# Optimization experiments

Measured on AMD Instinct MI355X. Metric: run time of the kernel, lower is better.

## Reference

```python
import jax, jax.numpy as jnp
import numpy as np
from jax import lax

T, B = 64, 16
N, W, R = 256, 64, 4          # mem_slot, mem_size, read_heads
IN, OUT = 64, 64
NHID, NNOUT = 256, 256
IF_SIZE = W * R + 3 * W + 5 * R + 3  # 471
EPS = 1e-6


def setup_inputs() -> dict:
    key = jax.random.key(0)
    ks = jax.random.split(key, 8)
    in_dim = IN + R * W
    def glorot(k, shape):
        fan_in = shape[0]
        return jax.random.normal(k, shape, dtype=jnp.float32) / np.sqrt(fan_in)
    return {
        "input_data": jax.random.normal(ks[0], (T, B, IN), dtype=jnp.float32),
        "W1": glorot(ks[1], (in_dim, NHID)),
        "b1": jnp.zeros((NHID,), jnp.float32),
        "W2": glorot(ks[2], (NHID, NNOUT)),
        "b2": jnp.zeros((NNOUT,), jnp.float32),
        "W_if": glorot(ks[3], (NNOUT, IF_SIZE)),
        "b_if": jnp.zeros((IF_SIZE,), jnp.float32),
        "W_out": glorot(ks[4], (NNOUT, OUT)),
        "W_mem_out": glorot(ks[5], (R * W, OUT)),
    }


def oneplus(x):
    return 1.0 + jax.nn.softplus(x)


def content_address(mem, keys, strengths):
    # mem [B,N,W], keys [B,W,R], strengths [B,R] -> weights [B,N,R]
    mem_n = mem / (jnp.linalg.norm(mem, axis=-1, keepdims=True) + EPS)
    key_n = keys / (jnp.linalg.norm(keys, axis=1, keepdims=True) + EPS)
    sim = jnp.einsum('bnw,bwr->bnr', mem_n, key_n)
    return jax.nn.softmax(sim * strengths[:, None, :], axis=1)


def parse_interface(z):
    # z: [B, IF_SIZE] -> dict of interface components (NeuCom layout)
    o = 0
    read_keys = z[:, o:o + W * R].reshape(-1, W, R); o += W * R
    read_str = oneplus(z[:, o:o + R]); o += R
    write_key = z[:, o:o + W]; o += W
    write_str = oneplus(z[:, o:o + 1]); o += 1
    erase = jax.nn.sigmoid(z[:, o:o + W]); o += W
    write_vec = z[:, o:o + W]; o += W
    free_gates = jax.nn.sigmoid(z[:, o:o + R]); o += R
    alloc_gate = jax.nn.sigmoid(z[:, o:o + 1]); o += 1
    write_gate = jax.nn.sigmoid(z[:, o:o + 1]); o += 1
    read_modes = jax.nn.softmax(z[:, o:o + 3 * R].reshape(-1, 3, R), axis=1)
    return (read_keys, read_str, write_key, write_str, erase, write_vec,
            free_gates, alloc_gate, write_gate, read_modes)


def _dnc_forward(input_data, W1, b1, W2, b2, W_if, b_if, W_out, W_mem_out):
    Bz = input_data.shape[1]
    eye = jnp.eye(N, dtype=input_data.dtype)

    def step(carry, x_t):
        mem, usage, rw, ww, prec, link, rvec = carry
        # --- controller (feedforward) ---
        ctrl_in = jnp.concatenate([x_t, rvec.reshape(Bz, R * W)], axis=1)
        h = jnp.tanh(ctrl_in @ W1 + b1)
        nn_out = jnp.tanh(h @ W2 + b2)
        (read_keys, read_str, write_key, write_str, erase, write_vec,
         free_gates, alloc_gate, write_gate, read_modes) = parse_interface(nn_out @ W_if + b_if)
        # --- write ---
        retention = jnp.prod(1.0 - free_gates[:, None, :] * rw, axis=2)   # [B,N]
        usage = (usage + ww - usage * ww) * retention
        idx = jnp.argsort(usage, axis=1)                                  # ascending usage
        u_sorted = jnp.take_along_axis(usage, idx, axis=1)
        prod_excl = jnp.concatenate(
            [jnp.ones((Bz, 1), usage.dtype), jnp.cumprod(u_sorted, axis=1)[:, :-1]], axis=1)
        alloc_sorted = (1.0 - u_sorted) * prod_excl
        alloc = jnp.take_along_axis(alloc_sorted, jnp.argsort(idx, axis=1), axis=1)
        wc = content_address(mem, write_key[:, :, None], write_str)[:, :, 0]  # [B,N]
        ww = write_gate * (alloc_gate * alloc + (1.0 - alloc_gate) * wc)
        mem = mem * (1.0 - ww[:, :, None] * erase[:, None, :]) \
              + ww[:, :, None] * write_vec[:, None, :]
        link = (1.0 - ww[:, :, None] - ww[:, None, :]) * link \
               + ww[:, :, None] * prec[:, None, :]
        link = link * (1.0 - eye)
        prec = (1.0 - jnp.sum(ww, axis=1, keepdims=True)) * prec + ww
        # --- read ---
        rc = content_address(mem, read_keys, read_str)                    # [B,N,R]
        fwd_w = jnp.einsum('bnm,bmr->bnr', link, rw)
        bwd_w = jnp.einsum('bmn,bmr->bnr', link, rw)
        rw = (bwd_w * read_modes[:, 0][:, None, :]
              + rc * read_modes[:, 1][:, None, :]
              + fwd_w * read_modes[:, 2][:, None, :])
        rvec = jnp.einsum('bnw,bnr->bwr', mem, rw)                        # [B,W,R]
        out = nn_out @ W_out + rvec.reshape(Bz, R * W) @ W_mem_out
        view = (free_gates, alloc_gate, write_gate, rw, ww, usage)
        return (mem, usage, rw, ww, prec, link, rvec), (out, view)

    carry0 = (
        jnp.full((Bz, N, W), EPS, input_data.dtype),   # mem_mat
        jnp.zeros((Bz, N), input_data.dtype),          # usage
        jnp.zeros((Bz, N, R), input_data.dtype),       # read_weight
        jnp.zeros((Bz, N), input_data.dtype),          # write_weight
        jnp.zeros((Bz, N), input_data.dtype),          # precedence
        jnp.zeros((Bz, N, N), input_data.dtype),       # link matrix
        jnp.zeros((Bz, W, R), input_data.dtype),       # read vectors
    )
    _, (outputs, _view) = lax.scan(step, carry0, input_data)
    return outputs  # [T,B,OUT]


def reference(input_data, W1, b1, W2, b2, W_if, b_if, W_out, W_mem_out):
    return _dnc_forward(input_data, W1, b1, W2, b2, W_if, b_if, W_out, W_mem_out)
```

## Files before the change

### kernel.cpp

```cpp
#include <hip/hip_runtime.h>
#include <hip/hip_fp16.h>
#include <math.h>

#define Tt 64
#define Bb 16
#define Nn 256
#define Ww 64
#define Rr 4
#define INd 64
#define OUTd 64
#define IFS 471
#define EPSf 1e-6f

#define W1OFF   0
#define W2OFF   40960
#define WIFOFF  73728
#define WOUTOFF 134016
#define WMEMOFF 142208
#define WTOT    150400

#define LROW    129
#define LINKB   (256 * LROW * 4)
#define SCRB    16384
#define FIXF    3824
#define SMEM_MAIN (LINKB + SCRB + FIXF * 4)
#define SMEM_FB   (SCRB + FIXF * 4)

typedef _Float16 h2v __attribute__((ext_vector_type(2)));
__device__ __forceinline__ float fdot2(__half2 a, __half2 b, float c) {
    return __builtin_amdgcn_fdot2(*(h2v*)&a, *(h2v*)&b, c, false);
}
__device__ __forceinline__ __half2 pkh(float a, float b) {
    auto r = __builtin_amdgcn_cvt_pkrtz(a, b);
    return *(__half2*)&r;
}

__device__ __forceinline__ float sigm(float x) { return 1.f / (1.f + expf(-x)); }
__device__ __forceinline__ float oneplus_(float x) {
    return 1.f + fmaxf(x, 0.f) + log1pf(expf(-fabsf(x)));
}
__device__ __forceinline__ float wsum(float v) {
#pragma unroll
    for (int o = 32; o; o >>= 1) v += __shfl_xor(v, o, 64);
    return v;
}
__device__ __forceinline__ float wmaxr(float v) {
#pragma unroll
    for (int o = 32; o; o >>= 1) v = fmaxf(v, __shfl_xor(v, o, 64));
    return v;
}

__device__ __attribute__((noinline)) float gemv_part(
    const __half2* __restrict__ wP, int str, int iters,
    const __half2* __restrict__ vin)
{
    float a[8] = {0.f,0.f,0.f,0.f,0.f,0.f,0.f,0.f};
#pragma unroll 1
    for (int j0 = 0; j0 < iters; j0 += 8) {
        __half2 hh[8], vv[8];
        int k8 = j0 >> 2;
        *(float4*)&hh[0] = *(const float4*)(wP + (size_t)k8 * str);
        *(float4*)&hh[4] = *(const float4*)(wP + (size_t)(k8 + 1) * str);
        *(float4*)&vv[0] = *(const float4*)(vin + j0);
        *(float4*)&vv[4] = *(const float4*)(vin + j0 + 4);
#pragma unroll
        for (int u = 0; u < 8; ++u) a[u] = fdot2(hh[u], vv[u], a[u]);
    }
    return ((a[0]+a[1])+(a[2]+a[3])) + ((a[4]+a[5])+(a[6]+a[7]));
}

__global__ void convert_weights(const float* __restrict__ W1, const float* __restrict__ W2,
                                const float* __restrict__ Wif, const float* __restrict__ Wout,
                                const float* __restrict__ Wmem, __half2* __restrict__ wp) {
    int i = blockIdx.x * blockDim.x + threadIdx.x;
    if (i >= WTOT) return;
    float a, b;
    if (i < W2OFF) {
        int q = i & 3, s = i >> 2, n = s & 255, k2 = (s >> 8) * 4 + q;
        a = W1[(2*k2)*256+n];  b = W1[(2*k2+1)*256+n];
    } else if (i < WIFOFF) {
        int t = i - W2OFF;
        int q = t & 3, s = t >> 2, n = s & 255, k2 = (s >> 8) * 4 + q;
        a = W2[(2*k2)*256+n];  b = W2[(2*k2+1)*256+n];
    } else if (i < WOUTOFF) {
        int t = i - WIFOFF;
        int q = t & 3, s = t >> 2, o = s % IFS, k2 = (s / IFS) * 4 + q;
        a = Wif[(2*k2)*IFS+o]; b = Wif[(2*k2+1)*IFS+o];
    } else if (i < WMEMOFF) {
        int t = i - WOUTOFF;
        int q = t & 3, s = t >> 2, n = s & 63, k2 = (s >> 6) * 4 + q;
        a = Wout[(2*k2)*64+n]; b = Wout[(2*k2+1)*64+n];
    } else {
        int t = i - WMEMOFF;
        int q = t & 3, s = t >> 2, n = s & 63, k2 = (s >> 6) * 4 + q;
        a = Wmem[(2*k2)*64+n]; b = Wmem[(2*k2+1)*64+n];
    }
    wp[i] = __floats2half2_rn(a, b);
}

template <bool LLINK>
__global__ __launch_bounds__(1024) void dnc_kernel(
    const float* __restrict__ x, const float* __restrict__ b1,
    const float* __restrict__ b2, const float* __restrict__ bif,
    const __half2* __restrict__ wp,
    __half* __restrict__ memg,
    __half2* __restrict__ linkg,
    float* __restrict__ out)
{
    extern __shared__ __align__(16) char smem[];
    const int b = blockIdx.x;
    const int tid = threadIdx.x;
    const int lane = tid & 63;
    const int wv = tid >> 6;

    __half2* l2p = (__half2*)smem;
    __half2* gl2 = linkg + (size_t)b * (256 * LROW);
    float* scr   = (float*)(smem + (LLINK ? LINKB : 0));
    __half* scrh = (__half*)scr;
    float* fx    = (float*)((char*)scr + SCRB);

    float*   s_rw    = fx + 0;
    __half2* s_ctrlh = (__half2*)(fx + 1024);
    __half2* s_hh    = (__half2*)(fx + 1184);
    __half2* s_nnh   = (__half2*)(fx + 1312);
    __half2* s_rwh   = (__half2*)(fx + 1440);
    float* s_z     = fx + 1952;
    float* s_usage = fx + 2424;
    float* s_ww    = fx + 2680;
    float* s_prec  = fx + 2936;
    float* s_wcdot = fx + 3192;
    float* s_wcss  = fx + 3448;
    float* s_knorm = fx + 3704;
    float* s_rstr  = fx + 3708;
    float* s_rmode = fx + 3712;
    float* s_sc    = fx + 3724;
    float* s_red   = fx + 3728;
    float* s_er    = fx + 3760;
    float* s_srt   = scr + 1024;
    float* s_cp    = scr + 1280;

    __half*  memh  = memg + (size_t)b * (Ww * Nn);
    __half2* memh2 = (__half2*)memh;

    auto lread = [&](int idx) -> __half2 {
        if constexpr (LLINK) return l2p[idx]; else return gl2[idx];
    };
    auto lwrite = [&](int idx, __half2 v) {
        if constexpr (LLINK) l2p[idx] = v; else gl2[idx] = v;
    };

    {
        __half2 z2 = pkh(0.f, 0.f);
#pragma unroll 1
        for (int i = tid; i < 256 * LROW; i += 1024) lwrite(i, z2);
        __half2 e2 = __floats2half2_rn(EPSf, EPSf);
#pragma unroll 1
        for (int j = 0; j < 8; ++j) memh2[tid + j * 1024] = e2;
        if (tid < 512) s_rwh[tid] = z2;
        if (tid < 32) {
            float2 xv = *(const float2*)&x[b * INd + 2 * tid];
            s_ctrlh[tid] = pkh(xv.x, xv.y);
        } else if (tid < 160) s_ctrlh[tid] = z2;
    }
    if (tid < 256) {
        s_usage[tid] = 0.f; s_ww[tid] = 0.f; s_prec[tid] = 0.f;
        s_rw[tid*4+0] = 0.f; s_rw[tid*4+1] = 0.f; s_rw[tid*4+2] = 0.f; s_rw[tid*4+3] = 0.f;
    }

#pragma unroll 1
    for (int t = 0; t < Tt; ++t) {
        __syncthreads();

        {
            int kc = wv >> 2, o = (wv & 3) * 64 + lane;
            scr[kc * 256 + o] = gemv_part(wp + W1OFF + o * 4 + kc * 10240, 1024, 40,
                                          s_ctrlh + kc * 40);
        }
        __syncthreads();
        if (tid < 256) {
            float v = tanhf(b1[tid] + ((scr[tid] + scr[256+tid]) + (scr[512+tid] + scr[768+tid])));
            float pv = __shfl_xor(v, 1, 64);
            if ((tid & 1) == 0) s_hh[tid >> 1] = pkh(v, pv);
        }
        __syncthreads();

        {
            int kc = wv >> 2, o = (wv & 3) * 64 + lane;
            scr[kc * 256 + o] = gemv_part(wp + W2OFF + o * 4 + kc * 8192, 1024, 32,
                                          s_hh + kc * 32);
        }
        __syncthreads();
        if (tid < 256) {
            float v = tanhf(b2[tid] + ((scr[tid] + scr[256+tid]) + (scr[512+tid] + scr[768+tid])));
            float pv = __shfl_xor(v, 1, 64);
            if ((tid & 1) == 0) s_nnh[tid >> 1] = pkh(v, pv);
        }
        __syncthreads();

        {
            int kc = wv >> 3, o = (wv & 7) * 64 + lane;
            if (o < IFS)
                scr[kc * 512 + o] = gemv_part(wp + WIFOFF + o * 4 + kc * 30144, 1884, 64,
                                              s_nnh + kc * 64);
        }
        __syncthreads();
        if (tid < IFS) s_z[tid] = bif[tid] + scr[tid] + scr[512 + tid];
        __syncthreads();

        if (wv < 4) {
            float vz = s_z[lane * 4 + wv];
            float s = wsum(vz * vz);
            if (lane == 0) s_knorm[wv] = sqrtf(s) + EPSf;
        } else if (wv == 4) {
            float vz = s_z[260 + lane];
            float s = wsum(vz * vz);
            if (lane == 0) s_sc[3] = sqrtf(s) + EPSf;
        } else if (wv == 5) {
            if (lane < 4) s_rstr[lane] = oneplus_(s_z[256 + lane]);
            else if (lane >= 8 && lane < 12) {
                int r = lane - 8;
                float a = s_z[459+r], bm = s_z[463+r], c = s_z[467+r];
                float mx = fmaxf(a, fmaxf(bm, c));
                float ea = expf(a-mx), eb = expf(bm-mx), ec = expf(c-mx);
                float inv = 1.f / ((ea+eb)+ec);
                s_rmode[0*4+r] = ea*inv; s_rmode[1*4+r] = eb*inv; s_rmode[2*4+r] = ec*inv;
            } else if (lane == 16) s_sc[0] = oneplus_(s_z[324]);
            else if (lane == 17) s_sc[1] = sigm(s_z[457]);
            else if (lane == 18) s_sc[2] = sigm(s_z[458]);
        } else if (wv == 6) {
            s_er[lane] = sigm(s_z[325 + lane]);
        } else if (wv >= 8 && wv < 12) {
            int n = tid - 512;
            float ret = 1.f;
#pragma unroll
            for (int r = 0; r < 4; ++r) {
                float fg = sigm(s_z[453 + r]);
                ret *= 1.f - fg * s_rw[n*4 + r];
            }
            float u = s_usage[n], wwo = s_ww[n];
            s_usage[n] = (u + wwo - u * wwo) * ret;
        } else if (wv >= 12) {
            int n = tid - 768;
            float dot = 0.f, ssv = 0.f;
#pragma unroll 1
            for (int w0 = 0; w0 < 64; w0 += 16) {
                __half hv[16];
#pragma unroll
                for (int u = 0; u < 16; ++u) hv[u] = memh[(w0 + u) * 256 + n];
#pragma unroll
                for (int u = 0; u < 16; ++u) {
                    float m = __half2float(hv[u]);
                    ssv = fmaf(m, m, ssv);
                    dot = fmaf(m, s_z[260 + w0 + u], dot);
                }
            }
            s_wcdot[n] = dot; s_wcss[n] = ssv;
        }
        __syncthreads();

        {
            int q = tid >> 8, n = tid & 255;
            float un = s_usage[n];
            float cnt = 0.f;
            int j0 = q * 64;
#pragma unroll 1
            for (int j = j0; j < j0 + 64; j += 4) {
                float4 uv = *(const float4*)&s_usage[j];
                cnt += (uv.x < un || (uv.x == un && j     < n)) ? 1.f : 0.f;
                cnt += (uv.y < un || (uv.y == un && j + 1 < n)) ? 1.f : 0.f;
                cnt += (uv.z < un || (uv.z == un && j + 2 < n)) ? 1.f : 0.f;
                cnt += (uv.w < un || (uv.w == un && j + 3 < n)) ? 1.f : 0.f;
            }
            scr[q * 256 + n] = cnt;
        }
        __syncthreads();

        if (wv == 0) {
            int rk[4]; float uu[4];
#pragma unroll
            for (int i = 0; i < 4; ++i) {
                int n = lane * 4 + i;
                float c = scr[n] + scr[256+n] + scr[512+n] + scr[768+n];
                rk[i] = (int)(c + 0.5f);
                uu[i] = s_usage[n];
                s_srt[rk[i]] = uu[i];
            }
            float4 vs = ((const float4*)s_srt)[lane];
            float p1 = vs.x * vs.y, p2 = p1 * vs.z, tot = p2 * vs.w;
            float incl = tot;
#pragma unroll
            for (int off = 1; off < 64; off <<= 1) {
                float tv = __shfl_up(incl, off, 64);
                if (lane >= off) incl *= tv;
            }
            float excl = __shfl_up(incl, 1, 64);
            if (lane == 0) excl = 1.f;
            float4 o4v; o4v.x = excl; o4v.y = excl*vs.x; o4v.z = excl*p1; o4v.w = excl*p2;
            ((float4*)s_cp)[lane] = o4v;

            float sims[4], mx = -1e30f;
#pragma unroll
            for (int i = 0; i < 4; ++i) {
                int n = lane * 4 + i;
                sims[i] = s_wcdot[n] / ((sqrtf(s_wcss[n]) + EPSf) * s_sc[3]) * s_sc[0];
                mx = fmaxf(mx, sims[i]);
            }
            mx = wmaxr(mx);
            float es[4], ls = 0.f;
#pragma unroll
            for (int i = 0; i < 4; ++i) { es[i] = expf(sims[i] - mx); ls += es[i]; }
            ls = wsum(ls);
            float ag = s_sc[1], wg = s_sc[2], inv = 1.f / ls, lw = 0.f;
#pragma unroll
            for (int i = 0; i < 4; ++i) {
                int n = lane * 4 + i;
                float alloc = (1.f - uu[i]) * s_cp[rk[i]];
                float wwn = wg * (ag * alloc + (1.f - ag) * es[i] * inv);
                s_ww[n] = wwn; lw += wwn;
            }
            lw = wsum(lw);
            if (lane == 0) s_red[0] = lw;
        }
        __syncthreads();

        if (tid < 512) {
            int kc = tid >> 7, p = tid & 127;
            int c0 = 2 * p, c1 = c0 + 1;
            float wwc0 = s_ww[c0], wwc1 = s_ww[c1];
            float pt0 = s_prec[c0], pt1 = s_prec[c1];
            float acc[8] = {0,0,0,0,0,0,0,0};
            int kbase = kc * 64;
#pragma unroll 1
            for (int k0 = kbase; k0 < kbase + 64; k0 += 8) {
                __half2 lv[8];
#pragma unroll
                for (int u = 0; u < 8; ++u) lv[u] = lread((k0 + u) * LROW + p);
                float wk8[8];
                *(float4*)&wk8[0] = *(const float4*)&s_ww[k0];
                *(float4*)&wk8[4] = *(const float4*)&s_ww[k0 + 4];
                float l0v[8], l1v[8];
#pragma unroll
                for (int u = 0; u < 8; ++u) {
                    int k = k0 + u;
                    float wk = wk8[u];
                    float2 lf = __half22float2(lv[u]);
                    float l0 = (1.f - wk - wwc0) * lf.x + wk * pt0;
                    float l1 = (1.f - wk - wwc1) * lf.y + wk * pt1;
                    if (k == c0) l0 = 0.f;
                    if (k == c1) l1 = 0.f;
                    l0v[u] = l0; l1v[u] = l1;
                }
#pragma unroll
                for (int u = 0; u < 8; ++u)
                    lwrite((k0 + u) * LROW + p, pkh(l0v[u], l1v[u]));
                __half2 l0p[4], l1p[4];
#pragma unroll
                for (int i = 0; i < 4; ++i) {
                    l0p[i] = pkh(l0v[2*i], l0v[2*i+1]);
                    l1p[i] = pkh(l1v[2*i], l1v[2*i+1]);
                }
                int kp0 = k0 >> 1;
#pragma unroll
                for (int r = 0; r < 4; ++r) {
                    __half2 rp[4];
                    *(float4*)rp = *(const float4*)(s_rwh + r * 128 + kp0);
#pragma unroll
                    for (int i = 0; i < 4; ++i) {
                        acc[r]     = fdot2(l0p[i], rp[i], acc[r]);
                        acc[4 + r] = fdot2(l1p[i], rp[i], acc[4 + r]);
                    }
                }
            }
            __half2* bp = (__half2*)scrh + (kc * 128 + p) * 4;
            bp[0] = pkh(acc[0], acc[1]);
            bp[1] = pkh(acc[2], acc[3]);
            bp[2] = pkh(acc[4], acc[5]);
            bp[3] = pkh(acc[6], acc[7]);
        } else {
            int t0 = tid - 512;
#pragma unroll 1
            for (int jb = 0; jb < 2; ++jb) {
                __half2 mv[8];
#pragma unroll
                for (int j = 0; j < 8; ++j) mv[j] = memh2[t0 + (jb * 8 + j) * 512];
#pragma unroll
                for (int j = 0; j < 8; ++j) {
                    int i2 = t0 + (jb * 8 + j) * 512;
                    int w = i2 >> 7, n2 = i2 & 127;
                    float er = s_er[w];
                    float wvv = s_z[389 + w];
                    float2 mf = __half22float2(mv[j]);
                    float wa = s_ww[2*n2], wb = s_ww[2*n2 + 1];
                    mf.x = mf.x * (1.f - wa * er) + wa * wvv;
                    mf.y = mf.y * (1.f - wb * er) + wb * wvv;
                    memh2[i2] = __floats2half2_rn(mf.x, mf.y);
                }
            }
        }
        __syncthreads();

        {
            int q = tid >> 8, n8 = tid & 255;
            float f[4] = {0.f, 0.f, 0.f, 0.f};
            int base = n8 * LROW + q * 32;
#pragma unroll 1
            for (int j0 = 0; j0 < 32; j0 += 8) {
                __half2 lv[8];
#pragma unroll
                for (int u = 0; u < 8; ++u) lv[u] = lread(base + j0 + u);
#pragma unroll
                for (int r = 0; r < 4; ++r) {
                    __half2 rp[8];
                    *(float4*)&rp[0] = *(const float4*)(s_rwh + r * 128 + q * 32 + j0);
                    *(float4*)&rp[4] = *(const float4*)(s_rwh + r * 128 + q * 32 + j0 + 4);
#pragma unroll
                    for (int u = 0; u < 8; ++u) f[r] = fdot2(lv[u], rp[u], f[r]);
                }
            }
            __half2* fp2 = (__half2*)(scrh + 4096) + (q * 256 + n8) * 2;
            fp2[0] = pkh(f[0], f[1]);
            fp2[1] = pkh(f[2], f[3]);
            if (q == 0) s_prec[n8] = (1.f - s_red[0]) * s_prec[n8] + s_ww[n8];
        }
        __syncthreads();

        int rr = tid >> 8, n8c = tid & 255;
        float bwv = 0.f, fwv = 0.f, e_rc = 0.f;
        {
#pragma unroll
            for (int kc = 0; kc < 4; ++kc)
                bwv += __half2float(scrh[(kc * 128 + (n8c >> 1)) * 8 + (n8c & 1) * 4 + rr]);
#pragma unroll
            for (int qq = 0; qq < 4; ++qq)
                fwv += __half2float(scrh[4096 + (qq * 256 + n8c) * 4 + rr]);
            float ssv = 0.f, dv = 0.f;
#pragma unroll 1
            for (int w0 = 0; w0 < 64; w0 += 16) {
                __half hv[16];
#pragma unroll
                for (int u = 0; u < 16; ++u) hv[u] = memh[(w0 + u) * 256 + n8c];
#pragma unroll
                for (int u = 0; u < 16; ++u) {
                    float m = __half2float(hv[u]);
                    ssv = fmaf(m, m, ssv);
                    dv = fmaf(m, s_z[(w0 + u) * 4 + rr], dv);
                }
            }
            float sim = dv / ((sqrtf(ssv) + EPSf) * s_knorm[rr]) * s_rstr[rr];
            e_rc = expf(sim);
            float s = wsum(e_rc);
            if (lane == 0) s_red[16 + wv] = s;
        }
        __syncthreads();
        {
            float sm = (s_red[16+rr*4+0] + s_red[16+rr*4+1]) + (s_red[16+rr*4+2] + s_red[16+rr*4+3]);
            float rc = e_rc / sm;
            float v = bwv * s_rmode[0*4+rr] + rc * s_rmode[1*4+rr] + fwv * s_rmode[2*4+rr];
            s_rw[n8c*4 + rr] = v;
            float pv = __shfl_xor(v, 1, 64);
            if ((n8c & 1) == 0) s_rwh[rr * 128 + (n8c >> 1)] = pkh(v, pv);
        }
        __syncthreads();

        {
            int kc = tid >> 8, o = tid & 255, w = o >> 2, r = o & 3;
            const __half2* mw2 = (const __half2*)(memh + w * 256 + kc * 64);
            const __half2* rw2 = s_rwh + r * 128 + kc * 32;
            float a = 0.f;
#pragma unroll
            for (int c = 0; c < 8; ++c) {
                __half2 mv[4], rv[4];
                *(float4*)mv = *(const float4*)(mw2 + c * 4);
                *(float4*)rv = *(const float4*)(rw2 + c * 4);
#pragma unroll
                for (int u = 0; u < 4; ++u) a = fdot2(mv[u], rv[u], a);
            }
            scr[kc * 256 + o] = a;
        }
        __syncthreads();

        if (tid < 256) {
            float v = (scr[tid] + scr[256+tid]) + (scr[512+tid] + scr[768+tid]);
            float pv = __shfl_xor(v, 1, 64);
            if ((tid & 1) == 0) s_ctrlh[32 + (tid >> 1)] = pkh(v, pv);
        } else if (tid >= 512 && tid < 544) {
            if (t + 1 < Tt) {
                int i = tid - 512;
                float2 xv = *(const float2*)&x[((t + 1) * Bb + b) * INd + 2 * i];
                s_ctrlh[i] = pkh(xv.x, xv.y);
            }
        }
        __syncthreads();

        {
            int c4 = wv, o4 = lane;
            const __half2* wsrc = (c4 < 8) ? (wp + WOUTOFF + o4 * 4 + c4 * 1024)
                                           : (wp + WMEMOFF + o4 * 4 + (c4 - 8) * 1024);
            const __half2* vsrc = (c4 < 8) ? (s_nnh + c4 * 16)
                                           : (s_ctrlh + 32 + (c4 - 8) * 16);
            scr[c4 * 64 + o4] = gemv_part(wsrc, 256, 16, vsrc);
        }
        __syncthreads();
        if (tid < 64) {
            float s = 0.f;
#pragma unroll
            for (int g = 0; g < 16; ++g) s += scr[g * 64 + tid];
            out[(t * Bb + b) * OUTd + tid] = s;
        }
    }
}

extern "C" void kernel_launch(void* const* d_in, const int* in_sizes, int n_in,
                              void* d_out, int out_size, void* d_ws, size_t ws_size,
                              hipStream_t stream) {
    const float* x    = (const float*)d_in[0];
    const float* W1   = (const float*)d_in[1];
    const float* b1   = (const float*)d_in[2];
    const float* W2   = (const float*)d_in[3];
    const float* b2   = (const float*)d_in[4];
    const float* Wif  = (const float*)d_in[5];
    const float* bif  = (const float*)d_in[6];
    const float* Wout = (const float*)d_in[7];
    const float* Wmem = (const float*)d_in[8];
    float* out = (float*)d_out;

    char* ws = (char*)d_ws;
    __half2* wp    = (__half2*)ws;
    __half*  memg  = (__half*)(ws + 601600);
    __half2* linkg = (__half2*)(ws + 601600 + 524288);

    convert_weights<<<dim3((WTOT + 255) / 256), dim3(256), 0, stream>>>(W1, W2, Wif, Wout, Wmem, wp);

    hipError_t rc = hipFuncSetAttribute(
        reinterpret_cast<const void*>(&dnc_kernel<true>),
        hipFuncAttributeMaxDynamicSharedMemorySize, SMEM_MAIN);
    if (rc == hipSuccess) {
        dnc_kernel<true><<<dim3(Bb), dim3(1024), SMEM_MAIN, stream>>>(
            x, b1, b2, bif, wp, memg, linkg, out);
    } else {
        dnc_kernel<false><<<dim3(Bb), dim3(1024), SMEM_FB, stream>>>(
            x, b1, b2, bif, wp, memg, linkg, out);
    }
}
```

Measured before the change: 1.999 ms.

## Keep a W-pair-interleaved half2 copy of memory for packed content-addressing dots

Adds a second global copy of the memory matrix stored as half2 pairs along the word dimension, maintained alongside the original during the write update. The two content-addressing loops (write key and read keys) now read half2 pairs and use packed fdot2 for both the dot product and the squared norm, with keys pre-packed into shared half2 buffers. The read-weight half buffer stride is padded to avoid conflicts, and some scratch arrays move into the scratch region. This halves the number of memory loads and converts scalar FMAs in addressing, at the cost of extra global writes per step and a larger workspace.

Result: faster. 1.880 ms (-5.9%).

```diff
diff --git a/kernel.cpp b/kernel.cpp
--- a/kernel.cpp
+++ b/kernel.cpp
@@ -22,9 +22,11 @@
 #define LROW    129
 #define LINKB   (256 * LROW * 4)
 #define SCRB    16384
-#define FIXF    3824
+#define FIXF    3456
 #define SMEM_MAIN (LINKB + SCRB + FIXF * 4)
 #define SMEM_FB   (SCRB + FIXF * 4)
+
+#define RWS 132
 
 typedef _Float16 h2v __attribute__((ext_vector_type(2)));
 __device__ __forceinline__ float fdot2(__half2 a, __half2 b, float c) {
@@ -104,6 +106,7 @@
     const float* __restrict__ b2, const float* __restrict__ bif,
     const __half2* __restrict__ wp,
     __half* __restrict__ memg,
+    __half2* __restrict__ memWg,
     __half2* __restrict__ linkg,
     float* __restrict__ out)
 {
@@ -124,23 +127,27 @@
     __half2* s_hh    = (__half2*)(fx + 1184);
     __half2* s_nnh   = (__half2*)(fx + 1312);
     __half2* s_rwh   = (__half2*)(fx + 1440);
-    float* s_z     = fx + 1952;
-    float* s_usage = fx + 2424;
-    float* s_ww    = fx + 2680;
-    float* s_prec  = fx + 2936;
-    float* s_wcdot = fx + 3192;
-    float* s_wcss  = fx + 3448;
-    float* s_knorm = fx + 3704;
-    float* s_rstr  = fx + 3708;
-    float* s_rmode = fx + 3712;
-    float* s_sc    = fx + 3724;
-    float* s_red   = fx + 3728;
-    float* s_er    = fx + 3760;
+    float* s_z     = fx + 1968;
+    float* s_usage = fx + 2440;
+    float* s_ww    = fx + 2696;
+    float* s_prec  = fx + 2952;
+    float* s_knorm = fx + 3208;
+    float* s_rstr  = fx + 3212;
+    float* s_rmode = fx + 3216;
+    float* s_sc    = fx + 3228;
+    float* s_red   = fx + 3232;
+    float* s_er    = fx + 3264;
+    __half2* s_keyh = (__half2*)(fx + 3328);
     float* s_srt   = scr + 1024;
     float* s_cp    = scr + 1280;
+    __half2* s_keyw2 = (__half2*)(scr + 1280);
+    float* s_wcdot = scr + 1536;
+    float* s_wcss  = scr + 1792;
 
     __half*  memh  = memg + (size_t)b * (Ww * Nn);
     __half2* memh2 = (__half2*)memh;
+    __half2* memW2 = memWg + (size_t)b * (32 * 256);
+    __half*  memWh = (__half*)memW2;
 
     auto lread = [&](int idx) -> __half2 {
         if constexpr (LLINK) return l2p[idx]; else return gl2[idx];
@@ -155,8 +162,8 @@
         for (int i = tid; i < 256 * LROW; i += 1024) lwrite(i, z2);
         __half2 e2 = __floats2half2_rn(EPSf, EPSf);
 #pragma unroll 1
-        for (int j = 0; j < 8; ++j) memh2[tid + j * 1024] = e2;
-        if (tid < 512) s_rwh[tid] = z2;
+        for (int j = 0; j < 8; ++j) { memh2[tid + j * 1024] = e2; memW2[tid + j * 1024] = e2; }
+        if (tid < 528) s_rwh[tid] = z2;
         if (tid < 32) {
             float2 xv = *(const float2*)&x[b * INd + 2 * tid];
             s_ctrlh[tid] = pkh(xv.x, xv.y);
@@ -204,7 +211,19 @@
                                               s_nnh + kc * 64);
         }
         __syncthreads();
-        if (tid < IFS) s_z[tid] = bif[tid] + scr[tid] + scr[512 + tid];
+        if (tid < IFS) {
+            float v = bif[tid] + scr[tid] + scr[512 + tid];
+            s_z[tid] = v;
+            float pv1 = __shfl_xor(v, 1, 64);
+            float pv4 = __shfl_xor(v, 4, 64);
+            if (tid < 256) {
+                if ((tid & 4) == 0)
+                    s_keyh[(tid & 3) * 32 + (tid >> 3)] = pkh(v, pv4);
+            } else if (tid >= 260 && tid < 324) {
+                if ((tid & 1) == 0)
+                    s_keyw2[(tid - 260) >> 1] = pkh(v, pv1);
+            }
+        }
         __syncthreads();
 
         if (wv < 4) {
@@ -241,17 +260,19 @@
             s_usage[n] = (u + wwo - u * wwo) * ret;
         } else if (wv >= 12) {
             int n = tid - 768;
+            const __half2* mW = memW2 + n;
             float dot = 0.f, ssv = 0.f;
 #pragma unroll 1
-            for (int w0 = 0; w0 < 64; w0 += 16) {
-                __half hv[16];
-#pragma unroll
-                for (int u = 0; u < 16; ++u) hv[u] = memh[(w0 + u) * 256 + n];
-#pragma unroll
-                for (int u = 0; u < 16; ++u) {
-                    float m = __half2float(hv[u]);
-                    ssv = fmaf(m, m, ssv);
-                    dot = fmaf(m, s_z[260 + w0 + u], dot);
+            for (int c = 0; c < 32; c += 8) {
+                __half2 mv[8], kv[8];
+#pragma unroll
+                for (int u = 0; u < 8; ++u) mv[u] = mW[(c + u) * 256];
+                *(float4*)&kv[0] = *(const float4*)(s_keyw2 + c);
+                *(float4*)&kv[4] = *(const float4*)(s_keyw2 + c + 4);
+#pragma unroll
+                for (int u = 0; u < 8; ++u) {
+                    ssv = fdot2(mv[u], mv[u], ssv);
+                    dot = fdot2(mv[u], kv[u], dot);
                 }
             }
             s_wcdot[n] = dot; s_wcss[n] = ssv;
@@ -363,7 +384,7 @@
 #pragma unroll
                 for (int r = 0; r < 4; ++r) {
                     __half2 rp[4];
-                    *(float4*)rp = *(const float4*)(s_rwh + r * 128 + kp0);
+                    *(float4*)rp = *(const float4*)(s_rwh + r * RWS + kp0);
 #pragma unroll
                     for (int i = 0; i < 4; ++i) {
                         acc[r]     = fdot2(l0p[i], rp[i], acc[r]);
@@ -393,7 +414,11 @@
                     float wa = s_ww[2*n2], wb = s_ww[2*n2 + 1];
                     mf.x = mf.x * (1.f - wa * er) + wa * wvv;
                     mf.y = mf.y * (1.f - wb * er) + wb * wvv;
-                    memh2[i2] = __floats2half2_rn(mf.x, mf.y);
+                    __half2 hv = __floats2half2_rn(mf.x, mf.y);
+                    memh2[i2] = hv;
+                    int wb2 = (w >> 1) * 512 + 4 * n2 + (w & 1);
+                    memWh[wb2]     = __low2half(hv);
+                    memWh[wb2 + 2] = __high2half(hv);
                 }
             }
         }
@@ -411,8 +436,8 @@
 #pragma unroll
                 for (int r = 0; r < 4; ++r) {
                     __half2 rp[8];
-                    *(float4*)&rp[0] = *(const float4*)(s_rwh + r * 128 + q * 32 + j0);
-                    *(float4*)&rp[4] = *(const float4*)(s_rwh + r * 128 + q * 32 + j0 + 4);
+                    *(float4*)&rp[0] = *(const float4*)(s_rwh + r * RWS + q * 32 + j0);
+                    *(float4*)&rp[4] = *(const float4*)(s_rwh + r * RWS + q * 32 + j0 + 4);
 #pragma unroll
                     for (int u = 0; u < 8; ++u) f[r] = fdot2(lv[u], rp[u], f[r]);
                 }
@@ -433,17 +458,20 @@
 #pragma unroll
             for (int qq = 0; qq < 4; ++qq)
                 fwv += __half2float(scrh[4096 + (qq * 256 + n8c) * 4 + rr]);
+            const __half2* mW = memW2 + n8c;
+            const __half2* kh = s_keyh + rr * 32;
             float ssv = 0.f, dv = 0.f;
 #pragma unroll 1
-            for (int w0 = 0; w0 < 64; w0 += 16) {
-                __half hv[16];
-#pragma unroll
-                for (int u = 0; u < 16; ++u) hv[u] = memh[(w0 + u) * 256 + n8c];
-#pragma unroll
-                for (int u = 0; u < 16; ++u) {
-                    float m = __half2float(hv[u]);
-                    ssv = fmaf(m, m, ssv);
-                    dv = fmaf(m, s_z[(w0 + u) * 4 + rr], dv);
+            for (int c = 0; c < 32; c += 8) {
+                __half2 mv[8], kv[8];
+#pragma unroll
+                for (int u = 0; u < 8; ++u) mv[u] = mW[(c + u) * 256];
+                *(float4*)&kv[0] = *(const float4*)(kh + c);
+                *(float4*)&kv[4] = *(const float4*)(kh + c + 4);
+#pragma unroll
+                for (int u = 0; u < 8; ++u) {
+                    ssv = fdot2(mv[u], mv[u], ssv);
+                    dv  = fdot2(mv[u], kv[u], dv);
                 }
             }
             float sim = dv / ((sqrtf(ssv) + EPSf) * s_knorm[rr]) * s_rstr[rr];
@@ -458,14 +486,14 @@
             float v = bwv * s_rmode[0*4+rr] + rc * s_rmode[1*4+rr] + fwv * s_rmode[2*4+rr];
             s_rw[n8c*4 + rr] = v;
             float pv = __shfl_xor(v, 1, 64);
-            if ((n8c & 1) == 0) s_rwh[rr * 128 + (n8c >> 1)] = pkh(v, pv);
+            if ((n8c & 1) == 0) s_rwh[rr * RWS + (n8c >> 1)] = pkh(v, pv);
         }
         __syncthreads();
 
         {
             int kc = tid >> 8, o = tid & 255, w = o >> 2, r = o & 3;
             const __half2* mw2 = (const __half2*)(memh + w * 256 + kc * 64);
-            const __half2* rw2 = s_rwh + r * 128 + kc * 32;
+            const __half2* rw2 = s_rwh + r * RWS + kc * 32;
             float a = 0.f;
 #pragma unroll
             for (int c = 0; c < 8; ++c) {
@@ -527,7 +555,8 @@
     char* ws = (char*)d_ws;
     __half2* wp    = (__half2*)ws;
     __half*  memg  = (__half*)(ws + 601600);
-    __half2* linkg = (__half2*)(ws + 601600 + 524288);
+    __half2* memWg = (__half2*)(ws + 601600 + 524288);
+    __half2* linkg = (__half2*)(ws + 601600 + 524288 + 524288);
 
     convert_weights<<<dim3((WTOT + 255) / 256), dim3(256), 0, stream>>>(W1, W2, Wif, Wout, Wmem, wp);
 
@@ -536,9 +565,9 @@
         hipFuncAttributeMaxDynamicSharedMemorySize, SMEM_MAIN);
     if (rc == hipSuccess) {
         dnc_kernel<true><<<dim3(Bb), dim3(1024), SMEM_MAIN, stream>>>(
-            x, b1, b2, bif, wp, memg, linkg, out);
+            x, b1, b2, bif, wp, memg, memWg, linkg, out);
     } else {
         dnc_kernel<false><<<dim3(Bb), dim3(1024), SMEM_FB, stream>>>(
-            x, b1, b2, bif, wp, memg, linkg, out);
+            x, b1, b2, bif, wp, memg, memWg, linkg, out);
     }
 }
```
